# Kernel tuning notes

Hardware: AMD Instinct MI355X
Metric: run time of the kernel (lower is better)

Reference implementation:

```python
import jax, jax.numpy as jnp
import numpy as np

B, C_IN, H, W = 4, 256, 200, 176
A = 6            # anchors per location (3 sizes x 2 rotations)
NUM_CLS = 4      # 3 classes + background
K = 100
N_ANCH = A * H * W


def setup_inputs() -> dict:
    key = jax.random.key(0)
    k1, k2, k3, k4, k5, k6 = jax.random.split(key, 6)
    x = jax.random.normal(k1, (B, C_IN, H, W), dtype=jnp.float32)
    scale = 1.0 / np.sqrt(C_IN)
    cls_w = jax.random.normal(k2, (NUM_CLS * A, C_IN), dtype=jnp.float32) * scale
    cls_b = jnp.zeros((NUM_CLS * A,), dtype=jnp.float32)
    reg_w = jax.random.normal(k3, (7 * A, C_IN), dtype=jnp.float32) * scale * 0.1
    reg_b = jnp.zeros((7 * A,), dtype=jnp.float32)
    # anchors: [N,7] = (x, y, z, dx, dy, dz, ry) with strictly positive sizes
    xyz = jax.random.uniform(k4, (N_ANCH, 3), minval=-35.0, maxval=35.0)
    sizes = jax.random.uniform(k5, (N_ANCH, 3), minval=1.0, maxval=4.0)
    rot = jax.random.uniform(k6, (N_ANCH, 1), minval=-np.pi, maxval=np.pi)
    anchors = jnp.concatenate([xyz, sizes, rot], axis=-1).astype(jnp.float32)
    return {"x": x, "cls_w": cls_w, "cls_b": cls_b,
            "reg_w": reg_w, "reg_b": reg_b, "anchors": anchors}


def _decode(deltas, anchors):
    # SECOND-style residual box decoder.  deltas, anchors: [B, N, 7]
    xa, ya, za, dxa, dya, dza, ra = jnp.split(anchors, 7, axis=-1)
    xt, yt, zt, dxt, dyt, dzt, rt = jnp.split(deltas, 7, axis=-1)
    diag = jnp.sqrt(dxa * dxa + dya * dya)
    xg = xt * diag + xa
    yg = yt * diag + ya
    zg = zt * dza + za
    dxg = jnp.exp(dxt) * dxa
    dyg = jnp.exp(dyt) * dya
    dzg = jnp.exp(dzt) * dza
    rg = rt + ra
    return jnp.concatenate([xg, yg, zg, dxg, dyg, dzg, rg], axis=-1)


def reference(x, cls_w, cls_b, reg_w, reg_b, anchors):
    # 1x1 conv heads: [B,C_in,H,W] -> [B,C_out,H,W]
    cls_pred = jnp.einsum('bchw,oc->bohw', x, cls_w) + cls_b[None, :, None, None]
    reg_pred = jnp.einsum('bchw,oc->bohw', x, reg_w) + reg_b[None, :, None, None]
    # permute(0,2,3,1).reshape(B, num_anchors, -1)
    cls_pred = jnp.transpose(cls_pred, (0, 2, 3, 1)).reshape(B, N_ANCH, NUM_CLS)
    reg_pred = jnp.transpose(reg_pred, (0, 2, 3, 1)).reshape(B, N_ANCH, 7)
    batch_anchors = jnp.broadcast_to(anchors[None], (B, N_ANCH, 7))
    pred_bboxes = _decode(reg_pred, batch_anchors)
    pred_scores = jax.nn.softmax(cls_pred, axis=-1)
    # per-frame top-k over max foreground score (classes 1:)
    max_scores = jnp.max(pred_scores[..., 1:], axis=-1)      # [B, N]
    _, topk_inds = jax.lax.top_k(max_scores, K)              # [B, K]
    topk_bboxes = jnp.take_along_axis(pred_bboxes, topk_inds[..., None], axis=1)
    topk_scores = jnp.take_along_axis(pred_scores, topk_inds[..., None], axis=1)
    return (topk_scores, topk_bboxes)
```

## Files before the change

### kernel.cpp

```cpp
#include <hip/hip_runtime.h>

#define BB 4
#define CIN 256
#define HW 35200
#define AA 6
#define NANCH (AA * HW)
#define TOPK 100
#define NBIN 4096
#define BINBASE 28416
#define CAP 4096
#define SMAX 4096
#define TILES 138
#define ZEROWORDS (BB * NBIN + 16)

__device__ __forceinline__ unsigned sbin(unsigned bits) {
  int v = (int)(bits >> 15) - BINBASE;
  v = v < 0 ? 0 : v;
  v = v > (NBIN - 1) ? (NBIN - 1) : v;
  return (unsigned)v;
}

__device__ __forceinline__ float sc4(float4 l) {
  float m = fmaxf(fmaxf(l.x, l.y), fmaxf(l.z, l.w));
  float e0 = expf(l.x - m), e1 = expf(l.y - m);
  float e2 = expf(l.z - m), e3 = expf(l.w - m);
  return fmaxf(fmaxf(e1, e2), e3) / (e0 + e1 + e2 + e3);
}

#define FMA4(A, W, S)                                      \
  A.x = fmaf(S, W.x, A.x); A.y = fmaf(S, W.y, A.y);        \
  A.z = fmaf(S, W.z, A.z); A.w = fmaf(S, W.w, A.w);

__global__ __launch_bounds__(256) void k0_init(
    const float* __restrict__ cls_w, float* __restrict__ wt,
    unsigned int* __restrict__ zr) {
  int t = blockIdx.x * 256 + threadIdx.x;
  int stride = gridDim.x * 256;
  for (int i = t; i < ZEROWORDS; i += stride) zr[i] = 0u;
  for (int i = t; i < 24 * CIN; i += stride)
    wt[(i % CIN) * 24 + (i / CIN)] = cls_w[i];
}

__global__ __launch_bounds__(256, 4) void k1_scores(
    const float* __restrict__ x, const float* __restrict__ wt,
    const float* __restrict__ cls_b, unsigned int* __restrict__ hist,
    float* __restrict__ maxsc) {
  int bid = blockIdx.x;
  int b = bid / TILES, tile = bid % TILES;
  int tid = threadIdx.x;

  __shared__ unsigned lh[NBIN];
  for (int i = tid; i < NBIN; i += 256) lh[i] = 0;
  __syncthreads();

  int hwg = tile * 256 + tid;
  bool act = hwg < HW;
  int hwc = act ? hwg : (HW - 1);
  const float* xb = x + (size_t)b * CIN * HW + hwc;

  float4 a0 = make_float4(cls_b[0], cls_b[1], cls_b[2], cls_b[3]);
  float4 a1 = make_float4(cls_b[4], cls_b[5], cls_b[6], cls_b[7]);
  float4 a2 = make_float4(cls_b[8], cls_b[9], cls_b[10], cls_b[11]);
  float4 a3 = make_float4(cls_b[12], cls_b[13], cls_b[14], cls_b[15]);
  float4 a4 = make_float4(cls_b[16], cls_b[17], cls_b[18], cls_b[19]);
  float4 a5 = make_float4(cls_b[20], cls_b[21], cls_b[22], cls_b[23]);

#pragma unroll 1
  for (int cc = 0; cc < CIN; cc += 16) {
    float xv[16];
#pragma unroll
    for (int u = 0; u < 16; ++u)
      xv[u] = xb[(size_t)(cc + u) * HW];
#pragma unroll
    for (int u = 0; u < 16; ++u) {
      const float4* wr = (const float4*)(wt + (cc + u) * 24);
      float4 w0 = wr[0], w1 = wr[1], w2 = wr[2];
      float4 w3 = wr[3], w4 = wr[4], w5 = wr[5];
      float s = xv[u];
      FMA4(a0, w0, s) FMA4(a1, w1, s) FMA4(a2, w2, s)
      FMA4(a3, w3, s) FMA4(a4, w4, s) FMA4(a5, w5, s)
    }
  }

  if (act) {
    float s0 = sc4(a0), s1 = sc4(a1), s2 = sc4(a2);
    float s3 = sc4(a3), s4 = sc4(a4), s5 = sc4(a5);
    float* mp = maxsc + (size_t)b * NANCH + (size_t)hwg * 6u;
    mp[0] = s0; mp[1] = s1; mp[2] = s2; mp[3] = s3; mp[4] = s4; mp[5] = s5;
    atomicAdd(&lh[sbin(__float_as_uint(s0))], 1u);
    atomicAdd(&lh[sbin(__float_as_uint(s1))], 1u);
    atomicAdd(&lh[sbin(__float_as_uint(s2))], 1u);
    atomicAdd(&lh[sbin(__float_as_uint(s3))], 1u);
    atomicAdd(&lh[sbin(__float_as_uint(s4))], 1u);
    atomicAdd(&lh[sbin(__float_as_uint(s5))], 1u);
  }
  __syncthreads();
  unsigned* gh = hist + (size_t)b * NBIN;
  for (int i = tid; i < NBIN; i += 256) {
    unsigned c = lh[i];
    if (c) atomicAdd(&gh[i], c);
  }
}

__global__ __launch_bounds__(256) void k3_compact(
    const unsigned int* __restrict__ hist, const float* __restrict__ maxsc,
    unsigned int* __restrict__ cand_count, unsigned long long* __restrict__ cand) {
  int tid = threadIdx.x;
  unsigned p = blockIdx.x * 256u + tid;
  unsigned b = p / NANCH, n = p % NANCH;

  __shared__ unsigned seg[256];
  __shared__ unsigned shT;
  const unsigned* h = hist + (size_t)b * NBIN;
  unsigned r[16];
  unsigned s = 0;
#pragma unroll
  for (int i = 0; i < 16; ++i) { r[i] = h[tid * 16 + i]; s += r[i]; }
  seg[tid] = s;
  __syncthreads();
  for (int d = 1; d < 256; d <<= 1) {
    unsigned add = (tid + d < 256) ? seg[tid + d] : 0u;
    __syncthreads();
    seg[tid] += add;
    __syncthreads();
  }
  unsigned above = (tid < 255) ? seg[tid + 1] : 0u;
  if (above < TOPK && above + s >= TOPK) {
    unsigned c = above, T = 0;
    for (int i = 15; i >= 0; --i) {
      c += r[i];
      if (c >= TOPK) { T = tid * 16u + (unsigned)i; break; }
    }
    shT = T;
  }
  __syncthreads();
  unsigned T = shT;

  unsigned bits = __float_as_uint(maxsc[p]);
  bool pred = sbin(bits) >= T;
  unsigned long long mask = __ballot(pred);
  if (mask) {
    int lane = tid & 63;
    int leader = (int)__ffsll(mask) - 1;
    unsigned base = 0;
    if (lane == leader)
      base = atomicAdd(&cand_count[b], (unsigned)__popcll(mask));
    base = __shfl(base, leader, 64);
    if (pred) {
      unsigned pos = base + (unsigned)__popcll(mask & ((1ull << lane) - 1ull));
      if (pos < CAP)
        cand[(size_t)b * CAP + pos] =
            ((unsigned long long)bits << 32) | (unsigned)(~n);
    }
  }
}

__global__ __launch_bounds__(1024) void k4_sort(
    const unsigned long long* __restrict__ cand,
    const unsigned int* __restrict__ cand_count, unsigned int* __restrict__ topk) {
  int b = blockIdx.x, tid = threadIdx.x;
  __shared__ unsigned long long sh[SMAX];
  unsigned cnt = cand_count[b];
  if (cnt > CAP) cnt = CAP;
  unsigned S = 128;
  while (S < cnt) S <<= 1;
  for (unsigned t = tid; t < S; t += 1024)
    sh[t] = (t < cnt) ? cand[(size_t)b * CAP + t] : 0ULL;
  __syncthreads();
  for (unsigned kk = 2; kk <= S; kk <<= 1) {
    for (unsigned jj = kk >> 1; jj > 0; jj >>= 1) {
      for (unsigned t = tid; t < S; t += 1024) {
        unsigned ixj = t ^ jj;
        if (ixj > t) {
          unsigned long long a = sh[t], c = sh[ixj];
          bool sw = ((t & kk) == 0) ? (a < c) : (a > c);
          if (sw) { sh[t] = c; sh[ixj] = a; }
        }
      }
      __syncthreads();
    }
  }
  if (tid < TOPK)
    topk[b * TOPK + tid] = ~(unsigned)(sh[tid] & 0xFFFFFFFFULL);
}

__global__ __launch_bounds__(256) void k5_out(
    const float* __restrict__ x, const float* __restrict__ cls_w,
    const float* __restrict__ cls_b, const float* __restrict__ reg_w,
    const float* __restrict__ reg_b, const float* __restrict__ anchors,
    const unsigned int* __restrict__ topk, float* __restrict__ out) {
  int bk = blockIdx.x;
  int b = bk / TOPK, k = bk % TOPK;
  unsigned n = topk[b * TOPK + k];
  int a = (int)(n % AA);
  unsigned hw = n / AA;
  int tid = threadIdx.x;

  float xv = x[(size_t)b * CIN * HW + (size_t)tid * HW + hw];
  float part[11];
#pragma unroll
  for (int j = 0; j < 4; ++j) part[j] = xv * cls_w[(a * 4 + j) * CIN + tid];
#pragma unroll
  for (int j = 0; j < 7; ++j) part[4 + j] = xv * reg_w[(a * 7 + j) * CIN + tid];

#pragma unroll
  for (int j = 0; j < 11; ++j) {
    float v = part[j];
    for (int off = 32; off > 0; off >>= 1) v += __shfl_down(v, off, 64);
    part[j] = v;
  }
  __shared__ float red[4][11];
  int wave = tid >> 6, lane = tid & 63;
  if (lane == 0) {
#pragma unroll
    for (int j = 0; j < 11; ++j) red[wave][j] = part[j];
  }
  __syncthreads();
  if (tid == 0) {
    float tot[11];
#pragma unroll
    for (int j = 0; j < 11; ++j)
      tot[j] = red[0][j] + red[1][j] + red[2][j] + red[3][j];
    float l0 = tot[0] + cls_b[a * 4 + 0];
    float l1 = tot[1] + cls_b[a * 4 + 1];
    float l2 = tot[2] + cls_b[a * 4 + 2];
    float l3 = tot[3] + cls_b[a * 4 + 3];
    float m = fmaxf(fmaxf(l0, l1), fmaxf(l2, l3));
    float e0 = expf(l0 - m), e1 = expf(l1 - m);
    float e2 = expf(l2 - m), e3 = expf(l3 - m);
    float inv = 1.0f / (e0 + e1 + e2 + e3);
    float* os = out + ((size_t)b * TOPK + k) * 4;
    os[0] = e0 * inv; os[1] = e1 * inv; os[2] = e2 * inv; os[3] = e3 * inv;
    const float* an = anchors + (size_t)n * 7;
    float xa = an[0], ya = an[1], za = an[2];
    float dxa = an[3], dya = an[4], dza = an[5], ra = an[6];
    float xt = tot[4] + reg_b[a * 7 + 0];
    float yt = tot[5] + reg_b[a * 7 + 1];
    float zt = tot[6] + reg_b[a * 7 + 2];
    float dxt = tot[7] + reg_b[a * 7 + 3];
    float dyt = tot[8] + reg_b[a * 7 + 4];
    float dzt = tot[9] + reg_b[a * 7 + 5];
    float rt = tot[10] + reg_b[a * 7 + 6];
    float diag = sqrtf(dxa * dxa + dya * dya);
    float* ob = out + (size_t)BB * TOPK * 4 + ((size_t)b * TOPK + k) * 7;
    ob[0] = xt * diag + xa;
    ob[1] = yt * diag + ya;
    ob[2] = zt * dza + za;
    ob[3] = expf(dxt) * dxa;
    ob[4] = expf(dyt) * dya;
    ob[5] = expf(dzt) * dza;
    ob[6] = rt + ra;
  }
}

extern "C" void kernel_launch(void* const* d_in, const int* in_sizes, int n_in,
                              void* d_out, int out_size, void* d_ws, size_t ws_size,
                              hipStream_t stream) {
  const float* x       = (const float*)d_in[0];
  const float* cls_w   = (const float*)d_in[1];
  const float* cls_b   = (const float*)d_in[2];
  const float* reg_w   = (const float*)d_in[3];
  const float* reg_b   = (const float*)d_in[4];
  const float* anchors = (const float*)d_in[5];
  float* out = (float*)d_out;

  char* ws = (char*)d_ws;
  unsigned int* hist       = (unsigned int*)(ws);
  unsigned int* cand_count = (unsigned int*)(ws + 65536);
  unsigned int* topk       = (unsigned int*)(ws + 65664);
  float* wt                = (float*)(ws + 67712);
  unsigned long long* cand = (unsigned long long*)(ws + 92288);
  float* maxsc             = (float*)(ws + 223360);

  k0_init<<<80, 256, 0, stream>>>(cls_w, wt, hist);
  k1_scores<<<BB * TILES, 256, 0, stream>>>(x, wt, cls_b, hist, maxsc);
  k3_compact<<<(BB * NANCH) / 256, 256, 0, stream>>>(hist, maxsc, cand_count, cand);
  k4_sort<<<BB, 1024, 0, stream>>>(cand, cand_count, topk);
  k5_out<<<BB * TOPK, 256, 0, stream>>>(x, cls_w, cls_b, reg_w, reg_b, anchors,
                                        topk, out);
}
```

Measured before the change: 245.5 us.

## Stage x channels through double-buffered LDS with vectorized float4 prefetch

The 1x1 classification-conv kernel now loads 16 channel rows per stage with float4 global loads into a double-buffered LDS tile. It prefetches the next stage into registers while computing the current one, replacing per-thread scalar strided loads. The aim is fewer memory instructions and better latency hiding on the large input read. In exchange it adds 32KB of LDS, extra barriers, and a lower occupancy bound in launch_bounds (3 blocks instead of 4).

After: 298.7 us. +21.7%, slower.

```diff
diff --git a/kernel.cpp b/kernel.cpp
--- a/kernel.cpp
+++ b/kernel.cpp
@@ -41,7 +41,7 @@
     wt[(i % CIN) * 24 + (i / CIN)] = cls_w[i];
 }
 
-__global__ __launch_bounds__(256, 4) void k1_scores(
+__global__ __launch_bounds__(256, 3) void k1_scores(
     const float* __restrict__ x, const float* __restrict__ wt,
     const float* __restrict__ cls_b, unsigned int* __restrict__ hist,
     float* __restrict__ maxsc) {
@@ -50,13 +50,27 @@
   int tid = threadIdx.x;
 
   __shared__ unsigned lh[NBIN];
+  __shared__ float xs[2][16][256];
   for (int i = tid; i < NBIN; i += 256) lh[i] = 0;
-  __syncthreads();
-
-  int hwg = tile * 256 + tid;
-  bool act = hwg < HW;
-  int hwc = act ? hwg : (HW - 1);
-  const float* xb = x + (size_t)b * CIN * HW + hwc;
+
+  int hw0 = tile * 256;
+  int w = tid >> 6, l = tid & 63;
+  int colb = 4 * l;
+  int maxcolb = HW - hw0 - 4;
+  if (colb > maxcolb) colb = maxcolb;
+  const float* srow = x + (size_t)b * CIN * HW + hw0 + colb;
+
+  float4 r0, r1, r2, r3;
+#define STAGE_LOAD(C0)                                               \
+  r0 = *(const float4*)(srow + (size_t)((C0) + w * 4 + 0) * HW);     \
+  r1 = *(const float4*)(srow + (size_t)((C0) + w * 4 + 1) * HW);     \
+  r2 = *(const float4*)(srow + (size_t)((C0) + w * 4 + 2) * HW);     \
+  r3 = *(const float4*)(srow + (size_t)((C0) + w * 4 + 3) * HW);
+#define STAGE_WRITE(BUF)                                             \
+  *(float4*)&xs[BUF][w * 4 + 0][4 * l] = r0;                         \
+  *(float4*)&xs[BUF][w * 4 + 1][4 * l] = r1;                         \
+  *(float4*)&xs[BUF][w * 4 + 2][4 * l] = r2;                         \
+  *(float4*)&xs[BUF][w * 4 + 3][4 * l] = r3;
 
   float4 a0 = make_float4(cls_b[0], cls_b[1], cls_b[2], cls_b[3]);
   float4 a1 = make_float4(cls_b[4], cls_b[5], cls_b[6], cls_b[7]);
@@ -65,23 +79,35 @@
   float4 a4 = make_float4(cls_b[16], cls_b[17], cls_b[18], cls_b[19]);
   float4 a5 = make_float4(cls_b[20], cls_b[21], cls_b[22], cls_b[23]);
 
+  STAGE_LOAD(0)
+  STAGE_WRITE(0)
+  __syncthreads();
+
 #pragma unroll 1
-  for (int cc = 0; cc < CIN; cc += 16) {
+  for (int c = 0; c < 16; ++c) {
+    int buf = c & 1;
+    if (c < 15) { STAGE_LOAD((c + 1) * 16) }
     float xv[16];
 #pragma unroll
-    for (int u = 0; u < 16; ++u)
-      xv[u] = xb[(size_t)(cc + u) * HW];
+    for (int u = 0; u < 16; ++u) xv[u] = xs[buf][u][tid];
 #pragma unroll
     for (int u = 0; u < 16; ++u) {
-      const float4* wr = (const float4*)(wt + (cc + u) * 24);
+      const float4* wr = (const float4*)(wt + (c * 16 + u) * 24);
       float4 w0 = wr[0], w1 = wr[1], w2 = wr[2];
       float4 w3 = wr[3], w4 = wr[4], w5 = wr[5];
       float s = xv[u];
       FMA4(a0, w0, s) FMA4(a1, w1, s) FMA4(a2, w2, s)
       FMA4(a3, w3, s) FMA4(a4, w4, s) FMA4(a5, w5, s)
     }
-  }
-
+    __syncthreads();
+    if (c < 15) {
+      STAGE_WRITE(buf ^ 1)
+      __syncthreads();
+    }
+  }
+
+  int hwg = hw0 + tid;
+  bool act = hwg < HW;
   if (act) {
     float s0 = sc4(a0), s1 = sc4(a1), s2 = sc4(a2);
     float s3 = sc4(a3), s4 = sc4(a4), s5 = sc4(a5);
@@ -97,8 +123,8 @@
   __syncthreads();
   unsigned* gh = hist + (size_t)b * NBIN;
   for (int i = tid; i < NBIN; i += 256) {
-    unsigned c = lh[i];
-    if (c) atomicAdd(&gh[i], c);
+    unsigned cnum = lh[i];
+    if (cnum) atomicAdd(&gh[i], cnum);
   }
 }
 
```

## Split channel reduction across waves with float4 pixel loads and LDS reduction

Applied to the files above, without the earlier changes.

The score kernel now gives each wave a quarter of the input channels, and each lane handles four adjacent pixels using float4 loads. The weight loads are then reused across four pixels, which cuts weight traffic per FMA. The partial sums from the four waves are combined serially through a shared-memory array before the softmax and histogram step. In exchange, register pressure rises (96 accumulators per thread, occupancy hint lowered to 2), LDS use grows by about 28KB, and four extra barriers are added.

Measured after the change: 282.4 us. 1.15x slower.

```diff
diff --git a/kernel.cpp b/kernel.cpp
--- a/kernel.cpp
+++ b/kernel.cpp
@@ -41,7 +41,7 @@
     wt[(i % CIN) * 24 + (i / CIN)] = cls_w[i];
 }
 
-__global__ __launch_bounds__(256, 4) void k1_scores(
+__global__ __launch_bounds__(256, 2) void k1_scores(
     const float* __restrict__ x, const float* __restrict__ wt,
     const float* __restrict__ cls_b, unsigned int* __restrict__ hist,
     float* __restrict__ maxsc) {
@@ -50,55 +50,86 @@
   int tid = threadIdx.x;
 
   __shared__ unsigned lh[NBIN];
+  __shared__ __align__(16) float sacc[256][28];
   for (int i = tid; i < NBIN; i += 256) lh[i] = 0;
-  __syncthreads();
-
-  int hwg = tile * 256 + tid;
-  bool act = hwg < HW;
-  int hwc = act ? hwg : (HW - 1);
-  const float* xb = x + (size_t)b * CIN * HW + hwc;
-
-  float4 a0 = make_float4(cls_b[0], cls_b[1], cls_b[2], cls_b[3]);
-  float4 a1 = make_float4(cls_b[4], cls_b[5], cls_b[6], cls_b[7]);
-  float4 a2 = make_float4(cls_b[8], cls_b[9], cls_b[10], cls_b[11]);
-  float4 a3 = make_float4(cls_b[12], cls_b[13], cls_b[14], cls_b[15]);
-  float4 a4 = make_float4(cls_b[16], cls_b[17], cls_b[18], cls_b[19]);
-  float4 a5 = make_float4(cls_b[20], cls_b[21], cls_b[22], cls_b[23]);
+
+  int w = tid >> 6, l = tid & 63;
+  int hw0 = tile * 256;
+  int colb = 4 * l;
+  bool valid = (hw0 + colb + 3) < HW;
+  int colc = valid ? colb : (HW - hw0 - 4);
+  const float* xb = x + (size_t)b * CIN * HW + hw0 + colc;
+  int c0 = w * 64;
+
+  float4 acc[4][6];
+#pragma unroll
+  for (int h = 0; h < 4; ++h)
+#pragma unroll
+    for (int j = 0; j < 6; ++j) acc[h][j] = make_float4(0.f, 0.f, 0.f, 0.f);
+
+#define FMA_HW(H, S)                                                  \
+  FMA4(acc[H][0], w0, S) FMA4(acc[H][1], w1, S) FMA4(acc[H][2], w2, S) \
+  FMA4(acc[H][3], w3, S) FMA4(acc[H][4], w4, S) FMA4(acc[H][5], w5, S)
 
 #pragma unroll 1
-  for (int cc = 0; cc < CIN; cc += 16) {
-    float xv[16];
-#pragma unroll
-    for (int u = 0; u < 16; ++u)
-      xv[u] = xb[(size_t)(cc + u) * HW];
-#pragma unroll
-    for (int u = 0; u < 16; ++u) {
-      const float4* wr = (const float4*)(wt + (cc + u) * 24);
+  for (int cc = 0; cc < 64; cc += 8) {
+    float4 xq[8];
+#pragma unroll
+    for (int u = 0; u < 8; ++u)
+      xq[u] = *(const float4*)(xb + (size_t)(c0 + cc + u) * HW);
+#pragma unroll
+    for (int u = 0; u < 8; ++u) {
+      const float4* wr = (const float4*)(wt + (c0 + cc + u) * 24);
       float4 w0 = wr[0], w1 = wr[1], w2 = wr[2];
       float4 w3 = wr[3], w4 = wr[4], w5 = wr[5];
-      float s = xv[u];
-      FMA4(a0, w0, s) FMA4(a1, w1, s) FMA4(a2, w2, s)
-      FMA4(a3, w3, s) FMA4(a4, w4, s) FMA4(a5, w5, s)
-    }
-  }
-
+      FMA_HW(0, xq[u].x) FMA_HW(1, xq[u].y)
+      FMA_HW(2, xq[u].z) FMA_HW(3, xq[u].w)
+    }
+  }
+
+  for (int r = 0; r < 4; ++r) {
+    if (w == r && valid) {
+#pragma unroll
+      for (int h = 0; h < 4; ++h) {
+        float4* dst = (float4*)&sacc[colb + h][0];
+        if (r == 0) {
+#pragma unroll
+          for (int j = 0; j < 6; ++j) dst[j] = acc[h][j];
+        } else {
+#pragma unroll
+          for (int j = 0; j < 6; ++j) {
+            float4 t = dst[j];
+            t.x += acc[h][j].x; t.y += acc[h][j].y;
+            t.z += acc[h][j].z; t.w += acc[h][j].w;
+            dst[j] = t;
+          }
+        }
+      }
+    }
+    __syncthreads();
+  }
+
+  int hwg = hw0 + tid;
+  bool act = hwg < HW;
   if (act) {
-    float s0 = sc4(a0), s1 = sc4(a1), s2 = sc4(a2);
-    float s3 = sc4(a3), s4 = sc4(a4), s5 = sc4(a5);
+    const float4* bias4 = (const float4*)cls_b;
+    const float4* row = (const float4*)&sacc[tid][0];
     float* mp = maxsc + (size_t)b * NANCH + (size_t)hwg * 6u;
-    mp[0] = s0; mp[1] = s1; mp[2] = s2; mp[3] = s3; mp[4] = s4; mp[5] = s5;
-    atomicAdd(&lh[sbin(__float_as_uint(s0))], 1u);
-    atomicAdd(&lh[sbin(__float_as_uint(s1))], 1u);
-    atomicAdd(&lh[sbin(__float_as_uint(s2))], 1u);
-    atomicAdd(&lh[sbin(__float_as_uint(s3))], 1u);
-    atomicAdd(&lh[sbin(__float_as_uint(s4))], 1u);
-    atomicAdd(&lh[sbin(__float_as_uint(s5))], 1u);
+#pragma unroll
+    for (int j = 0; j < 6; ++j) {
+      float4 v = row[j];
+      float4 bb = bias4[j];
+      v.x += bb.x; v.y += bb.y; v.z += bb.z; v.w += bb.w;
+      float sc = sc4(v);
+      mp[j] = sc;
+      atomicAdd(&lh[sbin(__float_as_uint(sc))], 1u);
+    }
   }
   __syncthreads();
   unsigned* gh = hist + (size_t)b * NBIN;
   for (int i = tid; i < NBIN; i += 256) {
-    unsigned c = lh[i];
-    if (c) atomicAdd(&gh[i], c);
+    unsigned cnum = lh[i];
+    if (cnum) atomicAdd(&gh[i], cnum);
   }
 }
 
```
